# Performance work log

Hardware: AMD Instinct MI355X
Metric: run time of the kernel (lower is better)

The kernel has to match this reference:

```python
import jax, jax.numpy as jnp
import numpy as np

N_NODES = 200000
N_EDGES = 6400000
N_GRAPHS = 2000


def _linear_params(key, fan_in, fan_out):
    k1, k2 = jax.random.split(key)
    bound = 1.0 / np.sqrt(fan_in)
    W = jax.random.uniform(k1, (fan_in, fan_out), minval=-bound, maxval=bound, dtype=jnp.float32)
    b = jax.random.uniform(k2, (fan_out,), minval=-bound, maxval=bound, dtype=jnp.float32)
    return W, b


def setup_inputs() -> dict:
    key = jax.random.key(0)
    ks = jax.random.split(key, 12)
    x = jax.random.normal(ks[0], (N_NODES, 2), dtype=jnp.float32)
    edge_index = jax.random.randint(ks[1], (2, N_EDGES), 0, N_NODES, dtype=jnp.int32)
    batch = jnp.sort(jax.random.randint(ks[2], (N_NODES,), 0, N_GRAPHS, dtype=jnp.int32))
    W1a, b1a = _linear_params(ks[3], 2, 16)
    W1b, b1b = _linear_params(ks[4], 16, 16)
    W2a, b2a = _linear_params(ks[5], 16, 16)
    W2b, b2b = _linear_params(ks[6], 16, 16)
    W3a, b3a = _linear_params(ks[7], 16, 16)
    W3b, b3b = _linear_params(ks[8], 16, 16)
    Wl1, bl1 = _linear_params(ks[9], 16, 16)
    Wl2, bl2 = _linear_params(ks[10], 16, 1)
    return dict(x=x, edge_index=edge_index, batch=batch,
                W1a=W1a, b1a=b1a, W1b=W1b, b1b=b1b,
                W2a=W2a, b2a=b2a, W2b=W2b, b2b=b2b,
                W3a=W3a, b3a=b3a, W3b=W3b, b3b=b3b,
                Wl1=Wl1, bl1=bl1, Wl2=Wl2, bl2=bl2)


def _gin_conv(x, src, dst, Wa, ba, Wb, bb):
    # sum-aggregate neighbor features at destination nodes; eps = 0
    msgs = x[src]                                            # [E, d]
    aggr = jax.ops.segment_sum(msgs, dst, num_segments=N_NODES)  # [N, d]
    h = x + aggr
    h = jax.nn.relu(h @ Wa + ba)
    return h @ Wb + bb


def reference(x, edge_index, batch,
              W1a, b1a, W1b, b1b,
              W2a, b2a, W2b, b2b,
              W3a, b3a, W3b, b3b,
              Wl1, bl1, Wl2, bl2):
    src, dst = edge_index[0], edge_index[1]
    h = jax.nn.relu(_gin_conv(x, src, dst, W1a, b1a, W1b, b1b))
    h = jax.nn.relu(_gin_conv(h, src, dst, W2a, b2a, W2b, b2b))
    h = jax.nn.relu(_gin_conv(h, src, dst, W3a, b3a, W3b, b3b))
    g = jax.ops.segment_sum(h, batch, num_segments=N_GRAPHS)  # global_add_pool -> [G, 16]
    g = jax.nn.relu(g @ Wl1 + bl1)
    return g @ Wl2 + bl2                                      # [G, 1]
```

## Files before the change

### kernel.cpp

```cpp
#include <hip/hip_runtime.h>

#define N_NODES 200000
#define N_EDGES 6400000
#define N_GRAPHS 2000

#define MBSHIFT 11
#define NMB 98
#define MBCAP 67584
#define CHUNKA 4096
#define PBLKA 1563
#define CHUNKB 8192
#define PB 9

#define FSHIFT 7
#define NBUCK 1563
#define CAPF 4608

__device__ __forceinline__ float bf_lo(unsigned v) { return __uint_as_float(v << 16); }
__device__ __forceinline__ float bf_hi(unsigned v) { return __uint_as_float(v & 0xFFFF0000u); }
__device__ __forceinline__ unsigned pack_bf2(float lo, float hi) {
  unsigned a = __float_as_uint(lo), b = __float_as_uint(hi);
  a = (a + 0x7FFFu + ((a >> 16) & 1u)) >> 16;
  b = (b + 0x7FFFu + ((b >> 16) & 1u)) >> 16;
  return a | (b << 16);
}

__global__ __launch_bounds__(256) void init_cursors(int* __restrict__ gcurA,
                                                    int* __restrict__ gcur2) {
  int i = blockIdx.x * 256 + threadIdx.x;
  if (i < NMB) gcurA[i] = i * MBCAP;
  if (i < NMB * 16) gcur2[i] = i * CAPF;
}

__global__ __launch_bounds__(256) void partA(
    const int* __restrict__ src, const int* __restrict__ dst,
    int* __restrict__ gcurA, int* __restrict__ colA) {
  __shared__ int hist[NMB], base[NMB], lcur[NMB];
  __shared__ int sc[128];
  __shared__ int sorted[CHUNKA];
  int t = threadIdx.x;
  for (int i = t; i < NMB; i += 256) hist[i] = 0;
  __syncthreads();
  int e0 = blockIdx.x * CHUNKA;
  int cnt = N_EDGES - e0; if (cnt > CHUNKA) cnt = CHUNKA;
  for (int i = t; i < cnt; i += 256) atomicAdd(&hist[dst[e0 + i] >> MBSHIFT], 1);
  __syncthreads();
  if (t < 128) sc[t] = (t < NMB) ? hist[t] : 0;
  __syncthreads();
  for (int off = 1; off < 128; off <<= 1) {
    int v = (t < 128 && t >= off) ? sc[t - off] : 0;
    __syncthreads();
    if (t < 128) sc[t] += v;
    __syncthreads();
  }
  if (t < NMB) {
    lcur[t] = sc[t] - hist[t];
    base[t] = hist[t] ? atomicAdd(&gcurA[t], hist[t]) : 0;
  }
  __syncthreads();
  for (int i = t; i < cnt; i += 256) {
    int d = dst[e0 + i];
    int b = d >> MBSHIFT;
    int r = atomicAdd(&lcur[b], 1);
    sorted[r] = (src[e0 + i] << MBSHIFT) | (d & 2047);
  }
  __syncthreads();
  for (int i = t; i < cnt; i += 256) {
    int lo = 0, hi = NMB;
    while (lo < hi) { int mid = (lo + hi) >> 1; if (sc[mid] <= i) lo = mid + 1; else hi = mid; }
    int b = lo;
    int pos = base[b] + (i - (sc[b] - hist[b]));
    if (pos < (b + 1) * MBCAP) colA[pos] = sorted[i];
  }
}

__global__ __launch_bounds__(256) void partB(
    const int* __restrict__ gcurA, const int* __restrict__ colA,
    int* __restrict__ gcur2, int* __restrict__ col) {
  __shared__ int hist[16], base[16], lcur[16], excl[16], sc16[16];
  __shared__ int sorted[CHUNKB];
  int t = threadIdx.x;
  int mb = blockIdx.x / PB, j = blockIdx.x % PB;
  int mbbase = mb * MBCAP;
  int mbcnt = gcurA[mb] - mbbase; if (mbcnt > MBCAP) mbcnt = MBCAP;
  int c0 = j * CHUNKB;
  int cnt = mbcnt - c0;
  if (cnt > CHUNKB) cnt = CHUNKB;
  if (cnt < 0) cnt = 0;
  if (t < 16) hist[t] = 0;
  __syncthreads();
  const int* seg = colA + mbbase + c0;
  for (int i = t; i < cnt; i += 256) atomicAdd(&hist[(seg[i] & 2047) >> FSHIFT], 1);
  __syncthreads();
  if (t == 0) {
    int run = 0;
    for (int b = 0; b < 16; b++) { excl[b] = run; lcur[b] = run; run += hist[b]; sc16[b] = run; }
  }
  if (t < 16) base[t] = hist[t] ? atomicAdd(&gcur2[mb * 16 + t], hist[t]) : 0;
  __syncthreads();
  for (int i = t; i < cnt; i += 256) {
    int p = seg[i];
    int b = (p & 2047) >> FSHIFT;
    int r = atomicAdd(&lcur[b], 1);
    sorted[r] = ((p >> MBSHIFT) << FSHIFT) | (p & 127);
  }
  __syncthreads();
  for (int i = t; i < cnt; i += 256) {
    int lo = 0, hi = 16;
    while (lo < hi) { int mid = (lo + hi) >> 1; if (sc16[mid] <= i) lo = mid + 1; else hi = mid; }
    int b = lo;
    int pos = base[b] + (i - excl[b]);
    if (pos < (mb * 16 + b + 1) * CAPF) col[pos] = sorted[i];
  }
}

__global__ __launch_bounds__(256) void sort_fine(
    const int* __restrict__ gcur2, int* __restrict__ col,
    int* __restrict__ rowstart, int* __restrict__ rowcnt) {
  __shared__ int hist[128], sc[128], lcur[128];
  __shared__ int sorted[CAPF];
  int t = threadIdx.x;
  int fb = blockIdx.x;
  int beg = fb * CAPF;
  int cnt = gcur2[fb] - beg; if (cnt > CAPF) cnt = CAPF;
  if (t < 128) hist[t] = 0;
  __syncthreads();
  for (int i = t; i < cnt; i += 256) atomicAdd(&hist[col[beg + i] & 127], 1);
  __syncthreads();
  if (t < 128) sc[t] = hist[t];
  __syncthreads();
  for (int off = 1; off < 128; off <<= 1) {
    int v = (t < 128 && t >= off) ? sc[t - off] : 0;
    __syncthreads();
    if (t < 128) sc[t] += v;
    __syncthreads();
  }
  if (t < 128) {
    int excl = sc[t] - hist[t];
    lcur[t] = excl;
    int n = fb * 128 + t;
    if (n < N_NODES) { rowstart[n] = beg + excl; rowcnt[n] = hist[t]; }
  }
  __syncthreads();
  for (int i = t; i < cnt; i += 256) {
    int p = col[beg + i];
    int r = atomicAdd(&lcur[p & 127], 1);
    sorted[r] = p >> FSHIFT;
  }
  __syncthreads();
  for (int i = t; i < cnt; i += 256) col[beg + i] = sorted[i];
}

__global__ __launch_bounds__(256) void aggr2_wave(
    const int* __restrict__ rowstart, const int* __restrict__ rowcnt,
    const int* __restrict__ col, const float* __restrict__ x,
    float* __restrict__ agg2) {
  int n = blockIdx.x * 8 + (threadIdx.x >> 5);
  int l32 = threadIdx.x & 31;
  int e0 = rowstart[n], c = rowcnt[n];
  float a0 = 0.f, a1 = 0.f;
  for (int idx = l32; idx < c; idx += 32) {
    int s = col[e0 + idx];
    float2 u = *reinterpret_cast<const float2*>(x + 2 * s);
    a0 += u.x; a1 += u.y;
  }
#pragma unroll
  for (int off = 1; off <= 16; off <<= 1) {
    a0 += __shfl_xor(a0, off, 64);
    a1 += __shfl_xor(a1, off, 64);
  }
  if (l32 == 0) {
    *reinterpret_cast<float2*>(agg2 + 2 * n) = make_float2(a0, a1);
  }
}

__global__ __launch_bounds__(256) void aggr16_wave(
    const int* __restrict__ rowstart, const int* __restrict__ rowcnt,
    const int* __restrict__ col, const uint4* __restrict__ hbf,
    float* __restrict__ agg) {
  int n = blockIdx.x * 4 + (threadIdx.x >> 6);
  int lane = threadIdx.x & 63;
  int e0 = rowstart[n], c = rowcnt[n];
  float a[8];
#pragma unroll
  for (int j = 0; j < 8; j++) a[j] = 0.f;
  int half = lane & 1;
  for (int idx = (lane >> 1); idx < c; idx += 32) {
    int s = col[e0 + idx];
    uint4 u = hbf[2 * s + half];
    a[0] += bf_lo(u.x); a[1] += bf_hi(u.x);
    a[2] += bf_lo(u.y); a[3] += bf_hi(u.y);
    a[4] += bf_lo(u.z); a[5] += bf_hi(u.z);
    a[6] += bf_lo(u.w); a[7] += bf_hi(u.w);
  }
#pragma unroll
  for (int off = 2; off <= 32; off <<= 1) {
#pragma unroll
    for (int j = 0; j < 8; j++) a[j] += __shfl_xor(a[j], off, 64);
  }
  if (lane < 2) {
    float* dstp = agg + (size_t)n * 16 + 8 * lane;
    *reinterpret_cast<float4*>(dstp)     = make_float4(a[0], a[1], a[2], a[3]);
    *reinterpret_cast<float4*>(dstp + 4) = make_float4(a[4], a[5], a[6], a[7]);
  }
}

__global__ __launch_bounds__(256) void node_l1(
    const float* __restrict__ x, const float* __restrict__ agg2,
    const float* __restrict__ Wa, const float* __restrict__ ba,
    const float* __restrict__ Wb, const float* __restrict__ bb,
    uint4* __restrict__ out) {
  __shared__ float sWa[32], sba[16], sWb[256], sbb[16];
  int t = threadIdx.x;
  if (t < 32) sWa[t] = Wa[t];
  if (t < 16) { sba[t] = ba[t]; sbb[t] = bb[t]; }
  for (int i = t; i < 256; i += 256) sWb[i] = Wb[i];
  __syncthreads();
  int n = blockIdx.x * blockDim.x + t;
  if (n >= N_NODES) return;
  float2 xv = *reinterpret_cast<const float2*>(x + 2 * n);
  float2 av = *reinterpret_cast<const float2*>(agg2 + 2 * n);
  float v0 = xv.x + av.x, v1 = xv.y + av.y;
  float h1[16];
#pragma unroll
  for (int j = 0; j < 16; j++)
    h1[j] = fmaxf(fmaf(v0, sWa[j], fmaf(v1, sWa[16 + j], sba[j])), 0.f);
  float o[16];
#pragma unroll
  for (int j = 0; j < 16; j++) {
    float s = sbb[j];
#pragma unroll
    for (int k = 0; k < 16; k++) s = fmaf(h1[k], sWb[k * 16 + j], s);
    o[j] = fmaxf(s, 0.f);
  }
  out[2 * n]     = make_uint4(pack_bf2(o[0], o[1]),  pack_bf2(o[2], o[3]),
                              pack_bf2(o[4], o[5]),  pack_bf2(o[6], o[7]));
  out[2 * n + 1] = make_uint4(pack_bf2(o[8], o[9]),  pack_bf2(o[10], o[11]),
                              pack_bf2(o[12], o[13]), pack_bf2(o[14], o[15]));
}

__global__ __launch_bounds__(256) void node16(
    const uint4* __restrict__ hin, const float* __restrict__ aggr,
    const float* __restrict__ Wa, const float* __restrict__ ba,
    const float* __restrict__ Wb, const float* __restrict__ bb,
    uint4* __restrict__ out) {
  __shared__ float sWa[256], sba[16], sWb[256], sbb[16];
  int t = threadIdx.x;
  if (t < 16) { sba[t] = ba[t]; sbb[t] = bb[t]; }
  for (int i = t; i < 256; i += 256) { sWa[i] = Wa[i]; sWb[i] = Wb[i]; }
  __syncthreads();
  int n = blockIdx.x * blockDim.x + t;
  if (n >= N_NODES) return;
  uint4 r0 = hin[2 * n], r1 = hin[2 * n + 1];
  const float4* ap = reinterpret_cast<const float4*>(aggr + 16 * n);
  float4 a0 = ap[0], a1 = ap[1], a2 = ap[2], a3 = ap[3];
  float v[16];
  v[0]  = bf_lo(r0.x) + a0.x;  v[1]  = bf_hi(r0.x) + a0.y;
  v[2]  = bf_lo(r0.y) + a0.z;  v[3]  = bf_hi(r0.y) + a0.w;
  v[4]  = bf_lo(r0.z) + a1.x;  v[5]  = bf_hi(r0.z) + a1.y;
  v[6]  = bf_lo(r0.w) + a1.z;  v[7]  = bf_hi(r0.w) + a1.w;
  v[8]  = bf_lo(r1.x) + a2.x;  v[9]  = bf_hi(r1.x) + a2.y;
  v[10] = bf_lo(r1.y) + a2.z;  v[11] = bf_hi(r1.y) + a2.w;
  v[12] = bf_lo(r1.z) + a3.x;  v[13] = bf_hi(r1.z) + a3.y;
  v[14] = bf_lo(r1.w) + a3.z;  v[15] = bf_hi(r1.w) + a3.w;
  float h1[16];
#pragma unroll
  for (int j = 0; j < 16; j++) {
    float s = sba[j];
#pragma unroll
    for (int k = 0; k < 16; k++) s = fmaf(v[k], sWa[k * 16 + j], s);
    h1[j] = fmaxf(s, 0.f);
  }
  float o[16];
#pragma unroll
  for (int j = 0; j < 16; j++) {
    float s = sbb[j];
#pragma unroll
    for (int k = 0; k < 16; k++) s = fmaf(h1[k], sWb[k * 16 + j], s);
    o[j] = fmaxf(s, 0.f);
  }
  out[2 * n]     = make_uint4(pack_bf2(o[0], o[1]),  pack_bf2(o[2], o[3]),
                              pack_bf2(o[4], o[5]),  pack_bf2(o[6], o[7]));
  out[2 * n + 1] = make_uint4(pack_bf2(o[8], o[9]),  pack_bf2(o[10], o[11]),
                              pack_bf2(o[12], o[13]), pack_bf2(o[14], o[15]));
}

__global__ __launch_bounds__(64) void pool_kernel(
    const uint4* __restrict__ h, const int* __restrict__ batch,
    float* __restrict__ g) {
  int gr = blockIdx.x;
  int lo = 0, hi = N_NODES;
  while (lo < hi) { int mid = (lo + hi) >> 1; if (batch[mid] < gr) lo = mid + 1; else hi = mid; }
  int start = lo;
  hi = N_NODES;
  while (lo < hi) { int mid = (lo + hi) >> 1; if (batch[mid] < gr + 1) lo = mid + 1; else hi = mid; }
  int end = lo;
  float acc[16];
#pragma unroll
  for (int j = 0; j < 16; j++) acc[j] = 0.f;
  for (int n = start + threadIdx.x; n < end; n += 64) {
    uint4 r0 = h[2 * n], r1 = h[2 * n + 1];
    acc[0]  += bf_lo(r0.x); acc[1]  += bf_hi(r0.x);
    acc[2]  += bf_lo(r0.y); acc[3]  += bf_hi(r0.y);
    acc[4]  += bf_lo(r0.z); acc[5]  += bf_hi(r0.z);
    acc[6]  += bf_lo(r0.w); acc[7]  += bf_hi(r0.w);
    acc[8]  += bf_lo(r1.x); acc[9]  += bf_hi(r1.x);
    acc[10] += bf_lo(r1.y); acc[11] += bf_hi(r1.y);
    acc[12] += bf_lo(r1.z); acc[13] += bf_hi(r1.z);
    acc[14] += bf_lo(r1.w); acc[15] += bf_hi(r1.w);
  }
#pragma unroll
  for (int j = 0; j < 16; j++) {
#pragma unroll
    for (int off = 32; off > 0; off >>= 1) acc[j] += __shfl_xor(acc[j], off, 64);
  }
  if (threadIdx.x == 0) {
    float4* gp = reinterpret_cast<float4*>(g + gr * 16);
#pragma unroll
    for (int q = 0; q < 4; q++)
      gp[q] = make_float4(acc[4 * q], acc[4 * q + 1], acc[4 * q + 2], acc[4 * q + 3]);
  }
}

__global__ __launch_bounds__(256) void head_kernel(
    const float* __restrict__ g,
    const float* __restrict__ Wl1, const float* __restrict__ bl1,
    const float* __restrict__ Wl2, const float* __restrict__ bl2,
    float* __restrict__ out) {
  __shared__ float sW1[256], sb1[16], sW2[16];
  int t = threadIdx.x;
  if (t < 16) { sb1[t] = bl1[t]; sW2[t] = Wl2[t]; }
  for (int i = t; i < 256; i += 256) sW1[i] = Wl1[i];
  __syncthreads();
  int gr = blockIdx.x * blockDim.x + t;
  if (gr >= N_GRAPHS) return;
  float v[16];
  const float4* gp = reinterpret_cast<const float4*>(g + 16 * gr);
#pragma unroll
  for (int q = 0; q < 4; q++) {
    float4 gv = gp[q];
    v[4 * q + 0] = gv.x; v[4 * q + 1] = gv.y; v[4 * q + 2] = gv.z; v[4 * q + 3] = gv.w;
  }
  float o = bl2[0];
#pragma unroll
  for (int j = 0; j < 16; j++) {
    float s = sb1[j];
#pragma unroll
    for (int k = 0; k < 16; k++) s = fmaf(v[k], sW1[k * 16 + j], s);
    o = fmaf(fmaxf(s, 0.f), sW2[j], o);
  }
  out[gr] = o;
}

extern "C" void kernel_launch(void* const* d_in, const int* in_sizes, int n_in,
                              void* d_out, int out_size, void* d_ws, size_t ws_size,
                              hipStream_t stream) {
  const float* x     = (const float*)d_in[0];
  const int*   ei    = (const int*)d_in[1];
  const int*   src   = ei;
  const int*   dst   = ei + N_EDGES;
  const int*   batch = (const int*)d_in[2];
  const float* W1a = (const float*)d_in[3];  const float* b1a = (const float*)d_in[4];
  const float* W1b = (const float*)d_in[5];  const float* b1b = (const float*)d_in[6];
  const float* W2a = (const float*)d_in[7];  const float* b2a = (const float*)d_in[8];
  const float* W2b = (const float*)d_in[9];  const float* b2b = (const float*)d_in[10];
  const float* W3a = (const float*)d_in[11]; const float* b3a = (const float*)d_in[12];
  const float* W3b = (const float*)d_in[13]; const float* b3b = (const float*)d_in[14];
  const float* Wl1 = (const float*)d_in[15]; const float* bl1 = (const float*)d_in[16];
  const float* Wl2 = (const float*)d_in[17]; const float* bl2 = (const float*)d_in[18];
  float* out = (float*)d_out;

  int*   gcurA    = (int*)d_ws;
  int*   gcur2    = gcurA + 128;
  int*   rowstart = gcur2 + 2048;
  int*   rowcnt   = rowstart + 200192;
  float* agg2     = (float*)(rowcnt + 200192);
  int*   col      = (int*)agg2 + 400384;
  int*   U        = col + (size_t)NBUCK * CAPF;
  int*   colA     = U;
  float* agg      = (float*)U;
  uint4* hA       = (uint4*)(agg + (size_t)N_NODES * 16);
  uint4* hB       = hA + (size_t)N_NODES * 2;
  float* g        = (float*)(hB + (size_t)N_NODES * 2);

  const int NWAVE_BLK = N_NODES / 4;
  const int N2_BLK = N_NODES / 8;
  dim3 ngrid((N_NODES + 255) / 256);

  init_cursors<<<(NMB * 16 + 255) / 256, 256, 0, stream>>>(gcurA, gcur2);
  partA<<<PBLKA, 256, 0, stream>>>(src, dst, gcurA, colA);
  partB<<<NMB * PB, 256, 0, stream>>>(gcurA, colA, gcur2, col);
  sort_fine<<<NBUCK, 256, 0, stream>>>(gcur2, col, rowstart, rowcnt);

  aggr2_wave<<<N2_BLK, 256, 0, stream>>>(rowstart, rowcnt, col, x, agg2);
  node_l1<<<ngrid, 256, 0, stream>>>(x, agg2, W1a, b1a, W1b, b1b, hA);
  aggr16_wave<<<NWAVE_BLK, 256, 0, stream>>>(rowstart, rowcnt, col, hA, agg);
  node16<<<ngrid, 256, 0, stream>>>(hA, agg, W2a, b2a, W2b, b2b, hB);
  aggr16_wave<<<NWAVE_BLK, 256, 0, stream>>>(rowstart, rowcnt, col, hB, agg);
  node16<<<ngrid, 256, 0, stream>>>(hB, agg, W3a, b3a, W3b, b3b, hA);

  pool_kernel<<<N_GRAPHS, 64, 0, stream>>>(hA, batch, g);
  head_kernel<<<(N_GRAPHS + 255) / 256, 256, 0, stream>>>(g, Wl1, bl1, Wl2, bl2, out);
}
```

Before: 365.5 us.

## Switch CSR aggregation from wave-per-node to lane-per-node gathers

Rewrites both gather-aggregation kernels so each node is handled by one lane (or a lane pair for 16-dim bf16 features), looping serially over its ~32 neighbors instead of spreading the neighbors across a wavefront and reducing with shuffles. This drops the cross-lane shuffle reductions and the mostly idle lanes during the write. In exchange, column-index reads are no longer coalesced across lanes, and degree imbalance between neighboring nodes causes divergence within a wave.

```diff
diff --git a/kernel.cpp b/kernel.cpp
--- a/kernel.cpp
+++ b/kernel.cpp
@@ -151,58 +151,45 @@
   for (int i = t; i < cnt; i += 256) col[beg + i] = sorted[i];
 }
 
-__global__ __launch_bounds__(256) void aggr2_wave(
+__global__ __launch_bounds__(256) void aggr2_lane(
     const int* __restrict__ rowstart, const int* __restrict__ rowcnt,
     const int* __restrict__ col, const float* __restrict__ x,
     float* __restrict__ agg2) {
-  int n = blockIdx.x * 8 + (threadIdx.x >> 5);
-  int l32 = threadIdx.x & 31;
+  int n = blockIdx.x * 256 + threadIdx.x;
+  if (n >= N_NODES) return;
   int e0 = rowstart[n], c = rowcnt[n];
   float a0 = 0.f, a1 = 0.f;
-  for (int idx = l32; idx < c; idx += 32) {
-    int s = col[e0 + idx];
+#pragma unroll 4
+  for (int i = 0; i < c; i++) {
+    int s = col[e0 + i];
     float2 u = *reinterpret_cast<const float2*>(x + 2 * s);
     a0 += u.x; a1 += u.y;
   }
-#pragma unroll
-  for (int off = 1; off <= 16; off <<= 1) {
-    a0 += __shfl_xor(a0, off, 64);
-    a1 += __shfl_xor(a1, off, 64);
-  }
-  if (l32 == 0) {
-    *reinterpret_cast<float2*>(agg2 + 2 * n) = make_float2(a0, a1);
-  }
-}
-
-__global__ __launch_bounds__(256) void aggr16_wave(
+  *reinterpret_cast<float2*>(agg2 + 2 * n) = make_float2(a0, a1);
+}
+
+__global__ __launch_bounds__(256) void aggr16_pair(
     const int* __restrict__ rowstart, const int* __restrict__ rowcnt,
     const int* __restrict__ col, const uint4* __restrict__ hbf,
     float* __restrict__ agg) {
-  int n = blockIdx.x * 4 + (threadIdx.x >> 6);
-  int lane = threadIdx.x & 63;
-  int e0 = rowstart[n], c = rowcnt[n];
-  float a[8];
-#pragma unroll
-  for (int j = 0; j < 8; j++) a[j] = 0.f;
-  int half = lane & 1;
-  for (int idx = (lane >> 1); idx < c; idx += 32) {
-    int s = col[e0 + idx];
+  int pn = blockIdx.x * 128 + (threadIdx.x >> 1);
+  int half = threadIdx.x & 1;
+  if (pn >= N_NODES) return;
+  int e0 = rowstart[pn], c = rowcnt[pn];
+  float a0 = 0.f, a1 = 0.f, a2 = 0.f, a3 = 0.f;
+  float a4 = 0.f, a5 = 0.f, a6 = 0.f, a7 = 0.f;
+#pragma unroll 4
+  for (int i = 0; i < c; i++) {
+    int s = col[e0 + i];
     uint4 u = hbf[2 * s + half];
-    a[0] += bf_lo(u.x); a[1] += bf_hi(u.x);
-    a[2] += bf_lo(u.y); a[3] += bf_hi(u.y);
-    a[4] += bf_lo(u.z); a[5] += bf_hi(u.z);
-    a[6] += bf_lo(u.w); a[7] += bf_hi(u.w);
-  }
-#pragma unroll
-  for (int off = 2; off <= 32; off <<= 1) {
-#pragma unroll
-    for (int j = 0; j < 8; j++) a[j] += __shfl_xor(a[j], off, 64);
-  }
-  if (lane < 2) {
-    float* dstp = agg + (size_t)n * 16 + 8 * lane;
-    *reinterpret_cast<float4*>(dstp)     = make_float4(a[0], a[1], a[2], a[3]);
-    *reinterpret_cast<float4*>(dstp + 4) = make_float4(a[4], a[5], a[6], a[7]);
-  }
+    a0 += bf_lo(u.x); a1 += bf_hi(u.x);
+    a2 += bf_lo(u.y); a3 += bf_hi(u.y);
+    a4 += bf_lo(u.z); a5 += bf_hi(u.z);
+    a6 += bf_lo(u.w); a7 += bf_hi(u.w);
+  }
+  float* dstp = agg + (size_t)pn * 16 + 8 * half;
+  *reinterpret_cast<float4*>(dstp)     = make_float4(a0, a1, a2, a3);
+  *reinterpret_cast<float4*>(dstp + 4) = make_float4(a4, a5, a6, a7);
 }
 
 __global__ __launch_bounds__(256) void node_l1(
@@ -383,20 +370,19 @@
   uint4* hB       = hA + (size_t)N_NODES * 2;
   float* g        = (float*)(hB + (size_t)N_NODES * 2);
 
-  const int NWAVE_BLK = N_NODES / 4;
-  const int N2_BLK = N_NODES / 8;
   dim3 ngrid((N_NODES + 255) / 256);
+  const int PAIR_BLK = (N_NODES + 127) / 128;
 
   init_cursors<<<(NMB * 16 + 255) / 256, 256, 0, stream>>>(gcurA, gcur2);
   partA<<<PBLKA, 256, 0, stream>>>(src, dst, gcurA, colA);
   partB<<<NMB * PB, 256, 0, stream>>>(gcurA, colA, gcur2, col);
   sort_fine<<<NBUCK, 256, 0, stream>>>(gcur2, col, rowstart, rowcnt);
 
-  aggr2_wave<<<N2_BLK, 256, 0, stream>>>(rowstart, rowcnt, col, x, agg2);
+  aggr2_lane<<<ngrid, 256, 0, stream>>>(rowstart, rowcnt, col, x, agg2);
   node_l1<<<ngrid, 256, 0, stream>>>(x, agg2, W1a, b1a, W1b, b1b, hA);
-  aggr16_wave<<<NWAVE_BLK, 256, 0, stream>>>(rowstart, rowcnt, col, hA, agg);
+  aggr16_pair<<<PAIR_BLK, 256, 0, stream>>>(rowstart, rowcnt, col, hA, agg);
   node16<<<ngrid, 256, 0, stream>>>(hA, agg, W2a, b2a, W2b, b2b, hB);
-  aggr16_wave<<<NWAVE_BLK, 256, 0, stream>>>(rowstart, rowcnt, col, hB, agg);
+  aggr16_pair<<<PAIR_BLK, 256, 0, stream>>>(rowstart, rowcnt, col, hB, agg);
   node16<<<ngrid, 256, 0, stream>>>(hB, agg, W3a, b3a, W3b, b3b, hA);
 
   pool_kernel<<<N_GRAPHS, 64, 0, stream>>>(hA, batch, g);
```

Result: slower. 392.5 us (+7.4%).

## Cache partition inputs in registers and scatter partB directly without LDS staging

Applied to the files above, without the earlier changes.

The three counting-sort passes (partA, partB, sort_fine) now load their input elements once into registers, using int4 vector loads where they can, instead of reading global memory twice for the histogram and the scatter. partB also drops its shared-memory sorted buffer and binary search and writes each element straight to its global slot from an atomic local cursor. The aim is to cut redundant global reads and LDS traffic in graph preprocessing. In exchange, partB's global writes are less coalesced, element order within a bucket becomes nondeterministic, and the larger register arrays raise register pressure.

```diff
diff --git a/kernel.cpp b/kernel.cpp
--- a/kernel.cpp
+++ b/kernel.cpp
@@ -43,7 +43,24 @@
   __syncthreads();
   int e0 = blockIdx.x * CHUNKA;
   int cnt = N_EDGES - e0; if (cnt > CHUNKA) cnt = CHUNKA;
-  for (int i = t; i < cnt; i += 256) atomicAdd(&hist[dst[e0 + i] >> MBSHIFT], 1);
+  int pr[16], br[16];
+#pragma unroll
+  for (int k = 0; k < 4; k++) {
+    if (k * 1024 < cnt) {
+      int i = e0 + k * 1024 + t * 4;
+      int4 d4 = *reinterpret_cast<const int4*>(dst + i);
+      int4 s4 = *reinterpret_cast<const int4*>(src + i);
+      br[4*k+0] = d4.x >> MBSHIFT; pr[4*k+0] = (s4.x << MBSHIFT) | (d4.x & 2047);
+      br[4*k+1] = d4.y >> MBSHIFT; pr[4*k+1] = (s4.y << MBSHIFT) | (d4.y & 2047);
+      br[4*k+2] = d4.z >> MBSHIFT; pr[4*k+2] = (s4.z << MBSHIFT) | (d4.z & 2047);
+      br[4*k+3] = d4.w >> MBSHIFT; pr[4*k+3] = (s4.w << MBSHIFT) | (d4.w & 2047);
+      atomicAdd(&hist[br[4*k+0]], 1); atomicAdd(&hist[br[4*k+1]], 1);
+      atomicAdd(&hist[br[4*k+2]], 1); atomicAdd(&hist[br[4*k+3]], 1);
+    } else {
+      br[4*k+0] = -1; br[4*k+1] = -1; br[4*k+2] = -1; br[4*k+3] = -1;
+      pr[4*k+0] = 0;  pr[4*k+1] = 0;  pr[4*k+2] = 0;  pr[4*k+3] = 0;
+    }
+  }
   __syncthreads();
   if (t < 128) sc[t] = (t < NMB) ? hist[t] : 0;
   __syncthreads();
@@ -58,11 +75,13 @@
     base[t] = hist[t] ? atomicAdd(&gcurA[t], hist[t]) : 0;
   }
   __syncthreads();
-  for (int i = t; i < cnt; i += 256) {
-    int d = dst[e0 + i];
-    int b = d >> MBSHIFT;
-    int r = atomicAdd(&lcur[b], 1);
-    sorted[r] = (src[e0 + i] << MBSHIFT) | (d & 2047);
+#pragma unroll
+  for (int k = 0; k < 16; k++) {
+    int b = br[k];
+    if (b >= 0) {
+      int r = atomicAdd(&lcur[b], 1);
+      sorted[r] = pr[k];
+    }
   }
   __syncthreads();
   for (int i = t; i < cnt; i += 256) {
@@ -77,8 +96,7 @@
 __global__ __launch_bounds__(256) void partB(
     const int* __restrict__ gcurA, const int* __restrict__ colA,
     int* __restrict__ gcur2, int* __restrict__ col) {
-  __shared__ int hist[16], base[16], lcur[16], excl[16], sc16[16];
-  __shared__ int sorted[CHUNKB];
+  __shared__ int hist[16], base[16], lcur[16];
   int t = threadIdx.x;
   int mb = blockIdx.x / PB, j = blockIdx.x % PB;
   int mbbase = mb * MBCAP;
@@ -87,30 +105,48 @@
   int cnt = mbcnt - c0;
   if (cnt > CHUNKB) cnt = CHUNKB;
   if (cnt < 0) cnt = 0;
-  if (t < 16) hist[t] = 0;
+  if (t < 16) { hist[t] = 0; }
   __syncthreads();
   const int* seg = colA + mbbase + c0;
-  for (int i = t; i < cnt; i += 256) atomicAdd(&hist[(seg[i] & 2047) >> FSHIFT], 1);
-  __syncthreads();
-  if (t == 0) {
-    int run = 0;
-    for (int b = 0; b < 16; b++) { excl[b] = run; lcur[b] = run; run += hist[b]; sc16[b] = run; }
-  }
-  if (t < 16) base[t] = hist[t] ? atomicAdd(&gcur2[mb * 16 + t], hist[t]) : 0;
-  __syncthreads();
-  for (int i = t; i < cnt; i += 256) {
-    int p = seg[i];
-    int b = (p & 2047) >> FSHIFT;
-    int r = atomicAdd(&lcur[b], 1);
-    sorted[r] = ((p >> MBSHIFT) << FSHIFT) | (p & 127);
-  }
-  __syncthreads();
-  for (int i = t; i < cnt; i += 256) {
-    int lo = 0, hi = 16;
-    while (lo < hi) { int mid = (lo + hi) >> 1; if (sc16[mid] <= i) lo = mid + 1; else hi = mid; }
-    int b = lo;
-    int pos = base[b] + (i - excl[b]);
-    if (pos < (mb * 16 + b + 1) * CAPF) col[pos] = sorted[i];
+  int pr[32];
+#pragma unroll
+  for (int k = 0; k < 8; k++) {
+    int i = k * 1024 + t * 4;
+    if (i + 3 < cnt) {
+      int4 v = *reinterpret_cast<const int4*>(seg + i);
+      pr[4*k+0] = v.x; pr[4*k+1] = v.y; pr[4*k+2] = v.z; pr[4*k+3] = v.w;
+      atomicAdd(&hist[(v.x & 2047) >> FSHIFT], 1);
+      atomicAdd(&hist[(v.y & 2047) >> FSHIFT], 1);
+      atomicAdd(&hist[(v.z & 2047) >> FSHIFT], 1);
+      atomicAdd(&hist[(v.w & 2047) >> FSHIFT], 1);
+    } else {
+#pragma unroll
+      for (int q = 0; q < 4; q++) {
+        int i2 = i + q;
+        if (i2 < cnt) {
+          int p = seg[i2];
+          pr[4*k+q] = p;
+          atomicAdd(&hist[(p & 2047) >> FSHIFT], 1);
+        } else pr[4*k+q] = -1;
+      }
+    }
+  }
+  __syncthreads();
+  if (t < 16) {
+    base[t] = hist[t] ? atomicAdd(&gcur2[mb * 16 + t], hist[t]) : 0;
+    lcur[t] = 0;
+  }
+  __syncthreads();
+#pragma unroll
+  for (int k = 0; k < 32; k++) {
+    int p = pr[k];
+    if (p >= 0) {
+      int b = (p & 2047) >> FSHIFT;
+      int r = atomicAdd(&lcur[b], 1);
+      int pos = base[b] + r;
+      if (pos < (mb * 16 + b + 1) * CAPF)
+        col[pos] = ((p >> MBSHIFT) << FSHIFT) | (p & 127);
+    }
   }
 }
 
@@ -125,7 +161,14 @@
   int cnt = gcur2[fb] - beg; if (cnt > CAPF) cnt = CAPF;
   if (t < 128) hist[t] = 0;
   __syncthreads();
-  for (int i = t; i < cnt; i += 256) atomicAdd(&hist[col[beg + i] & 127], 1);
+  int pr[18];
+#pragma unroll
+  for (int k = 0; k < 18; k++) {
+    int i = k * 256 + t;
+    int p = (i < cnt) ? col[beg + i] : -1;
+    pr[k] = p;
+    if (p >= 0) atomicAdd(&hist[p & 127], 1);
+  }
   __syncthreads();
   if (t < 128) sc[t] = hist[t];
   __syncthreads();
@@ -142,10 +185,13 @@
     if (n < N_NODES) { rowstart[n] = beg + excl; rowcnt[n] = hist[t]; }
   }
   __syncthreads();
-  for (int i = t; i < cnt; i += 256) {
-    int p = col[beg + i];
-    int r = atomicAdd(&lcur[p & 127], 1);
-    sorted[r] = p >> FSHIFT;
+#pragma unroll
+  for (int k = 0; k < 18; k++) {
+    int p = pr[k];
+    if (p >= 0) {
+      int r = atomicAdd(&lcur[p & 127], 1);
+      sorted[r] = p >> FSHIFT;
+    }
   }
   __syncthreads();
   for (int i = t; i < cnt; i += 256) col[beg + i] = sorted[i];
```

After: 340.3 us (median of 2 runs). 1.07x faster.
